# Optimization experiments

Measured on AMD Instinct MI355X. Metric: run time of the kernel, lower is better.

## Reference

```python
import jax, jax.numpy as jnp
import numpy as np

PH, PW = 7, 7            # output_size
SCALE = 0.25             # spatial_scale
SR = 2                   # sampling_ratio (fixed, jit-static)
ALIGNED = True


def setup_inputs() -> dict:
    key = jax.random.key(0)
    k1, k2, k3, k4, k5 = jax.random.split(key, 5)
    B, C, H, W = 4, 256, 200, 200
    N = 512
    img = H / SCALE  # 800.0 image size
    x = jax.random.normal(k1, (B, C, H, W), dtype=jnp.float32)
    bidx = jax.random.randint(k2, (N,), 0, B).astype(jnp.float32)
    cxy = jax.random.uniform(k3, (N, 2), minval=0.0, maxval=img)
    wh = jax.random.uniform(k4, (N, 2), minval=32.0, maxval=256.0)
    x1y1 = jnp.clip(cxy - wh / 2, 0.0, img - 1.0)
    x2y2 = jnp.clip(cxy + wh / 2, 0.0, img - 1.0)
    rois = jnp.concatenate([bidx[:, None], x1y1[:, 0:1], x1y1[:, 1:2],
                            x2y2[:, 0:1], x2y2[:, 1:2]], axis=1).astype(jnp.float32)
    return {"input": x, "rois": rois}


def _axis_samples(start, bin_size, P, size):
    """Sample coords along one axis. start/bin_size: [N]. Returns per-sample
    low/high integer indices, interp weights, and validity mask, all [N, P*SR]."""
    ib = jnp.arange(P, dtype=jnp.float32)           # bin index
    isr = jnp.arange(SR, dtype=jnp.float32)         # sample within bin
    # coord[n, p, s] = start + p*bin + (s+0.5)*bin/SR
    coord = (start[:, None, None]
             + ib[None, :, None] * bin_size[:, None, None]
             + (isr[None, None, :] + 0.5) * bin_size[:, None, None] / SR)
    coord = coord.reshape(coord.shape[0], P * SR)
    valid = (coord >= -1.0) & (coord <= size)
    c = jnp.maximum(coord, 0.0)
    lo_raw = jnp.floor(c).astype(jnp.int32)
    at_edge = lo_raw >= size - 1
    lo = jnp.where(at_edge, size - 1, lo_raw)
    hi = jnp.where(at_edge, size - 1, lo_raw + 1)
    cv = jnp.where(at_edge, jnp.float32(size - 1), c)
    frac = cv - lo.astype(jnp.float32)              # weight toward hi
    return lo, hi, frac, valid


def reference(input, rois):
    B, C, H, W = input.shape
    N = rois.shape[0]
    b = rois[:, 0].astype(jnp.int32)
    off = 0.5 if ALIGNED else 0.0
    sx = rois[:, 1] * SCALE - off
    sy = rois[:, 2] * SCALE - off
    ex = rois[:, 3] * SCALE - off
    ey = rois[:, 4] * SCALE - off
    rw, rh = ex - sx, ey - sy
    if not ALIGNED:
        rw = jnp.maximum(rw, 1.0)
        rh = jnp.maximum(rh, 1.0)
    bin_w, bin_h = rw / PW, rh / PH

    yl, yh, fy, vy = _axis_samples(sy, bin_h, PH, H)   # [N, Sy]
    xl, xh, fx, vx = _axis_samples(sx, bin_w, PW, W)   # [N, Sx]

    featT = jnp.transpose(input, (0, 2, 3, 1))         # [B,H,W,C]

    def gather(yi, xi):  # -> [N, Sy, Sx, C]
        return featT[b[:, None, None], yi[:, :, None], xi[:, None, :]]

    hy, ly = (1.0 - fy), fy
    hx, lx = (1.0 - fx), fx
    w_ll = (hy[:, :, None] * hx[:, None, :])[..., None]
    w_lh = (hy[:, :, None] * lx[:, None, :])[..., None]
    w_hl = (ly[:, :, None] * hx[:, None, :])[..., None]
    w_hh = (ly[:, :, None] * lx[:, None, :])[..., None]

    val = (w_ll * gather(yl, xl) + w_lh * gather(yl, xh)
           + w_hl * gather(yh, xl) + w_hh * gather(yh, xh))
    mask = (vy[:, :, None] & vx[:, None, :])[..., None]
    val = jnp.where(mask, val, 0.0)                    # [N, Sy, Sx, C]

    # average pool the SRxSR samples per output bin
    val = val.reshape(N, PH, SR, PW, SR, C).mean(axis=(2, 4))  # [N,PH,PW,C]
    return jnp.transpose(val, (0, 3, 1, 2))            # [N,C,PH,PW]
```

## Files before the change

### kernel.cpp

```cpp
#include <hip/hip_runtime.h>


#define R_PH 7
#define R_PW 7
#define R_SR 2
#define R_SCALE 0.25f
#define R_C 256
#define R_H 200
#define R_W 200
#define R_HW (R_H * R_W)
#define STRIP 50
#define NSTRIP 4
#define STAGE_ROWS 56

__device__ __forceinline__ void axis_sample(float start, float bin, int p, int s, int size,
                                            int& lo, int& hi, float& wlo, float& whi) {
    float coord = (start + (float)p * bin) + ((float)s + 0.5f) * bin * (1.0f / R_SR);
    bool valid = (coord >= -1.0f) && (coord <= (float)size);
    float c = fmaxf(coord, 0.0f);
    int lo_raw = (int)floorf(c);
    bool at_edge = lo_raw >= size - 1;
    lo = at_edge ? size - 1 : lo_raw;
    hi = at_edge ? size - 1 : lo_raw + 1;
    float cv = at_edge ? (float)(size - 1) : c;
    float frac = cv - (float)lo;
    whi = valid ? frac : 0.0f;
    wlo = valid ? (1.0f - frac) : 0.0f;
}

__global__ void __launch_bounds__(512)
build_lists(const float* __restrict__ rois, int N, int* __restrict__ ws) {
    __shared__ int lcnt[NSTRIP * 4];
    int t = threadIdx.x;
    if (t < 16) lcnt[t] = 0;
    __syncthreads();
    int* lists = ws + 16;
    for (int n = t; n < N; n += 512) {
        const float* r = rois + (size_t)n * 5;
        int b = (int)r[0];
        float sy = r[2] * R_SCALE - 0.5f;
        float ey = r[4] * R_SCALE - 0.5f;
        float binh = (ey - sy) * (1.0f / R_PH);
        for (int ph = 0; ph < R_PH; ++ph) {
            int lo, hi; float wl, wh;
            axis_sample(sy, binh, ph, 0, R_H, lo, hi, wl, wh);
            int bs = b * NSTRIP + lo / STRIP;
            int pos = atomicAdd(&lcnt[bs], 1);
            lists[bs * (N * R_PH) + pos] = (n << 3) | ph;
        }
    }
    __syncthreads();
    if (t < 16) ws[t] = lcnt[t];
}

__global__ void __launch_bounds__(512)
roi_strip(const float* __restrict__ input,
          const float* __restrict__ rois,
          const int* __restrict__ ws, int N,
          float* __restrict__ out) {
    __shared__ float pl[STAGE_ROWS * R_W];
    int c = blockIdx.x;
    int b = blockIdx.y;
    int s = blockIdx.z;

    int m = ws[b * NSTRIP + s];
    if (m == 0) return;

    int r0 = s * STRIP;
    int nrows = min(STAGE_ROWS, R_H - r0);

    const float* src = input + (size_t)(b * R_C + c) * R_HW + r0 * R_W;
    int nf4 = nrows * (R_W / 4);
    int tid = threadIdx.x;
    for (int base = 0; base < nf4; base += 512) {
        int i = base + tid;
        if (i < nf4) {
            __builtin_amdgcn_global_load_lds(
                (const __attribute__((address_space(1))) void*)(src + (size_t)i * 4),
                (__attribute__((address_space(3))) void*)(pl + (size_t)i * 4),
                16, 0, 0);
        }
    }

    const int* list = ws + 16 + (b * NSTRIP + s) * (N * R_PH);
    __syncthreads();

    int total = m * R_PW;
    for (int i = threadIdx.x; i < total; i += 512) {
        int e  = i / R_PW;
        int pw = i - e * R_PW;
        int code = list[e];
        int n  = code >> 3;
        int ph = code & 7;
        const float* r = rois + (size_t)n * 5;
        float sx = r[1] * R_SCALE - 0.5f;
        float sy = r[2] * R_SCALE - 0.5f;
        float ex = r[3] * R_SCALE - 0.5f;
        float ey = r[4] * R_SCALE - 0.5f;
        float binw = (ex - sx) * (1.0f / R_PW);
        float binh = (ey - sy) * (1.0f / R_PH);

        int   ylo[R_SR], yhi[R_SR], xlo[R_SR], xhi[R_SR];
        float wyl[R_SR], wyh[R_SR], wxl[R_SR], wxh[R_SR];
#pragma unroll
        for (int q = 0; q < R_SR; ++q) {
            axis_sample(sy, binh, ph, q, R_H, ylo[q], yhi[q], wyl[q], wyh[q]);
            axis_sample(sx, binw, pw, q, R_W, xlo[q], xhi[q], wxl[q], wxh[q]);
        }

        float acc = 0.0f;
#pragma unroll
        for (int ys = 0; ys < R_SR; ++ys) {
            const float* rlo = pl + (ylo[ys] - r0) * R_W;
            const float* rhi = pl + (yhi[ys] - r0) * R_W;
#pragma unroll
            for (int xs = 0; xs < R_SR; ++xs) {
                acc += wyl[ys] * (wxl[xs] * rlo[xlo[xs]] + wxh[xs] * rlo[xhi[xs]])
                     + wyh[ys] * (wxl[xs] * rhi[xlo[xs]] + wxh[xs] * rhi[xhi[xs]]);
            }
        }
        out[(size_t)(n * R_C + c) * 49 + ph * R_PW + pw] = acc * 0.25f;
    }
}

__global__ void __launch_bounds__(256)
roi_align_fwd(const float* __restrict__ input,
              const float* __restrict__ rois,
              float* __restrict__ out, int total) {
    int idx = blockIdx.x * blockDim.x + threadIdx.x;
    if (idx >= total) return;
    int pw = idx % R_PW;
    int ph = (idx / R_PW) % R_PH;
    int c  = (idx / (R_PW * R_PH)) % R_C;
    int n  = idx / (R_PW * R_PH * R_C);
    const float* r = rois + (size_t)n * 5;
    int   b  = (int)r[0];
    float sx = r[1] * R_SCALE - 0.5f;
    float sy = r[2] * R_SCALE - 0.5f;
    float ex = r[3] * R_SCALE - 0.5f;
    float ey = r[4] * R_SCALE - 0.5f;
    float bin_w = (ex - sx) * (1.0f / R_PW);
    float bin_h = (ey - sy) * (1.0f / R_PH);
    const float* plane = input + (size_t)(b * R_C + c) * R_HW;
    int   ylo[R_SR], yhi[R_SR], xlo[R_SR], xhi[R_SR];
    float wylo[R_SR], wyhi[R_SR], wxlo[R_SR], wxhi[R_SR];
#pragma unroll
    for (int s = 0; s < R_SR; ++s) {
        axis_sample(sy, bin_h, ph, s, R_H, ylo[s], yhi[s], wylo[s], wyhi[s]);
        axis_sample(sx, bin_w, pw, s, R_W, xlo[s], xhi[s], wxlo[s], wxhi[s]);
    }
    float acc = 0.0f;
#pragma unroll
    for (int ys = 0; ys < R_SR; ++ys) {
        const float* row_lo = plane + ylo[ys] * R_W;
        const float* row_hi = plane + yhi[ys] * R_W;
#pragma unroll
        for (int xs = 0; xs < R_SR; ++xs) {
            acc += wylo[ys] * (wxlo[xs] * row_lo[xlo[xs]] + wxhi[xs] * row_lo[xhi[xs]])
                 + wyhi[ys] * (wxlo[xs] * row_hi[xlo[xs]] + wxhi[xs] * row_hi[xhi[xs]]);
        }
    }
    out[idx] = acc * (1.0f / (R_SR * R_SR));
}

extern "C" void kernel_launch(void* const* d_in, const int* in_sizes, int n_in,
                              void* d_out, int out_size, void* d_ws, size_t ws_size,
                              hipStream_t stream) {
    const float* input = (const float*)d_in[0];
    const float* rois  = (const float*)d_in[1];
    float* out = (float*)d_out;
    int N = in_sizes[1] / 5;

    size_t ws_needed = (size_t)(16 + 16 * N * R_PH) * sizeof(int);
    if (ws_size >= ws_needed) {
        int* ws = (int*)d_ws;
        build_lists<<<1, 512, 0, stream>>>(rois, N, ws);
        dim3 grid(R_C, 4, NSTRIP);
        roi_strip<<<grid, 512, 0, stream>>>(input, rois, ws, N, out);
    } else {
        int total = out_size;
        roi_align_fwd<<<(total + 255) / 256, 256, 0, stream>>>(input, rois, out, total);
    }
}
```

Measured before the change: 257.4 us.

## Fuse per-strip ROI list construction into the strip kernel using shared memory

Removes the separate single-block build_lists launch and its global workspace. Each strip block now scans all ROIs itself, keeps those matching its batch and row strip, and builds a compact list in LDS with 16-bit codes, overlapping this scan with the async global-to-LDS staging of the feature rows. This drops a kernel launch and a serial dependency, at the cost of every block redundantly scanning all ROIs and extra LDS use.

```diff
diff --git a/kernel.cpp b/kernel.cpp
--- a/kernel.cpp
+++ b/kernel.cpp
@@ -12,6 +12,8 @@
 #define STRIP 50
 #define NSTRIP 4
 #define STAGE_ROWS 56
+#define MAXROI 512
+#define MAXE (MAXROI * R_PH)
 
 __device__ __forceinline__ void axis_sample(float start, float bin, int p, int s, int size,
                                             int& lo, int& hi, float& wlo, float& whi) {
@@ -29,49 +31,29 @@
 }
 
 __global__ void __launch_bounds__(512)
-build_lists(const float* __restrict__ rois, int N, int* __restrict__ ws) {
-    __shared__ int lcnt[NSTRIP * 4];
-    int t = threadIdx.x;
-    if (t < 16) lcnt[t] = 0;
-    __syncthreads();
-    int* lists = ws + 16;
-    for (int n = t; n < N; n += 512) {
-        const float* r = rois + (size_t)n * 5;
-        int b = (int)r[0];
-        float sy = r[2] * R_SCALE - 0.5f;
-        float ey = r[4] * R_SCALE - 0.5f;
-        float binh = (ey - sy) * (1.0f / R_PH);
-        for (int ph = 0; ph < R_PH; ++ph) {
-            int lo, hi; float wl, wh;
-            axis_sample(sy, binh, ph, 0, R_H, lo, hi, wl, wh);
-            int bs = b * NSTRIP + lo / STRIP;
-            int pos = atomicAdd(&lcnt[bs], 1);
-            lists[bs * (N * R_PH) + pos] = (n << 3) | ph;
-        }
-    }
-    __syncthreads();
-    if (t < 16) ws[t] = lcnt[t];
-}
-
-__global__ void __launch_bounds__(512)
-roi_strip(const float* __restrict__ input,
-          const float* __restrict__ rois,
-          const int* __restrict__ ws, int N,
+roi_fused(const float* __restrict__ input,
+          const float* __restrict__ rois, int N,
           float* __restrict__ out) {
     __shared__ float pl[STAGE_ROWS * R_W];
+    __shared__ unsigned short lst[MAXE];
+    __shared__ int lcnt;
     int c = blockIdx.x;
     int b = blockIdx.y;
     int s = blockIdx.z;
+    int tid = threadIdx.x;
 
-    int m = ws[b * NSTRIP + s];
-    if (m == 0) return;
+    if (tid == 0) lcnt = 0;
+    float f0 = 0.f, f2 = 0.f, f4 = 0.f;
+    if (tid < N) {
+        const float* r = rois + (size_t)tid * 5;
+        f0 = r[0]; f2 = r[2]; f4 = r[4];
+    }
+    __syncthreads();
 
     int r0 = s * STRIP;
     int nrows = min(STAGE_ROWS, R_H - r0);
-
     const float* src = input + (size_t)(b * R_C + c) * R_HW + r0 * R_W;
     int nf4 = nrows * (R_W / 4);
-    int tid = threadIdx.x;
     for (int base = 0; base < nf4; base += 512) {
         int i = base + tid;
         if (i < nf4) {
@@ -82,14 +64,33 @@
         }
     }
 
-    const int* list = ws + 16 + (b * NSTRIP + s) * (N * R_PH);
+    for (int n = tid; n < N; n += 512) {
+        float a0, a2, a4;
+        if (n == tid) { a0 = f0; a2 = f2; a4 = f4; }
+        else { const float* r = rois + (size_t)n * 5; a0 = r[0]; a2 = r[2]; a4 = r[4]; }
+        if ((int)a0 == b) {
+            float sy = a2 * R_SCALE - 0.5f;
+            float ey = a4 * R_SCALE - 0.5f;
+            float binh = (ey - sy) * (1.0f / R_PH);
+            for (int ph = 0; ph < R_PH; ++ph) {
+                int lo, hi; float wl, wh;
+                axis_sample(sy, binh, ph, 0, R_H, lo, hi, wl, wh);
+                if (lo / STRIP == s) {
+                    int pos = atomicAdd(&lcnt, 1);
+                    lst[pos] = (unsigned short)((n << 3) | ph);
+                }
+            }
+        }
+    }
+
     __syncthreads();
+    int m = lcnt;
 
     int total = m * R_PW;
-    for (int i = threadIdx.x; i < total; i += 512) {
+    for (int i = tid; i < total; i += 512) {
         int e  = i / R_PW;
         int pw = i - e * R_PW;
-        int code = list[e];
+        int code = lst[e];
         int n  = code >> 3;
         int ph = code & 7;
         const float* r = rois + (size_t)n * 5;
@@ -171,12 +172,9 @@
     float* out = (float*)d_out;
     int N = in_sizes[1] / 5;
 
-    size_t ws_needed = (size_t)(16 + 16 * N * R_PH) * sizeof(int);
-    if (ws_size >= ws_needed) {
-        int* ws = (int*)d_ws;
-        build_lists<<<1, 512, 0, stream>>>(rois, N, ws);
+    if (N <= MAXROI) {
         dim3 grid(R_C, 4, NSTRIP);
-        roi_strip<<<grid, 512, 0, stream>>>(input, rois, ws, N, out);
+        roi_fused<<<grid, 512, 0, stream>>>(input, rois, N, out);
     } else {
         int total = out_size;
         roi_align_fwd<<<(total + 255) / 256, 256, 0, stream>>>(input, rois, out, total);
```

New measurement: 253.0 us. About the same (-1.7%).
